# Optimization experiments

Hardware: AMD Instinct MI355X
Metric: run time of the kernel (lower is better)

## Reference

```python
import jax, jax.numpy as jnp
import numpy as np

N = 8192
INP_DIM = 512
OUT_DIM = 256


def setup_inputs() -> dict:
    key = jax.random.key(0)
    k1, k2, k3, k4, k5 = jax.random.split(key, 5)
    x = jax.random.normal(k1, (N, INP_DIM), dtype=jnp.float32)
    adj = jax.random.uniform(k2, (N, N), dtype=jnp.float32)  # threshold at 0.5 below
    # learned params: w ~ torch.rand(inp_dim, out_dim); Linear(out_dim, out_dim)
    w = jax.random.uniform(k3, (INP_DIM, OUT_DIM), dtype=jnp.float32)
    bound = 1.0 / np.sqrt(OUT_DIM)
    lin_w = jax.random.uniform(k4, (OUT_DIM, OUT_DIM), minval=-bound, maxval=bound, dtype=jnp.float32)
    lin_b = jax.random.uniform(k5, (OUT_DIM,), minval=-bound, maxval=bound, dtype=jnp.float32)
    return {"x": x, "adj": adj, "w": w, "lin_w": lin_w, "lin_b": lin_b}


def reference(x, adj, w, lin_w, lin_b):
    n = adj.shape[0]
    # A = binarize(adj) + I
    A = jnp.where(adj > 0.5, 1.0, 0.0) + jnp.eye(n, dtype=adj.dtype)
    # D is diagonal, so inverse().sqrt() == diag(1/sqrt(deg)); deg >= 1 from self-loops
    d_inv_sqrt = jax.lax.rsqrt(jnp.sum(A, axis=1))  # [N]
    # A_hat = D^{-1/2} A D^{-1/2} as row/col scaling (same math, O(N^2))
    A_hat = A * d_inv_sqrt[:, None] * d_inv_sqrt[None, :]
    # message passing + feature transform
    h = jax.nn.relu((A_hat @ x) @ w)           # [N, out_dim]
    return h @ lin_w.T + lin_b                  # Linear(out_dim, out_dim)
```

## Files before the change

### kernel.cpp

```cpp
#include <hip/hip_runtime.h>
#include <hip/hip_bf16.h>

typedef __attribute__((ext_vector_type(4))) float f32x4;
typedef __attribute__((ext_vector_type(8))) short s16x8;
typedef unsigned int uint;
typedef unsigned short ushort;
typedef unsigned long long u64;


__device__ inline ushort f2bf(float f) {
  union { float f; uint u; } v; v.f = f;
  uint r = (v.u + 0x7FFFu + ((v.u >> 16) & 1u)) >> 16;
  return (ushort)r;
}
__device__ inline float bf2f(ushort h) { union { uint u; float f; } v; v.u = ((uint)h) << 16; return v.f; }
__device__ inline uint pack2(float a, float b) { return (uint)f2bf(a) | ((uint)f2bf(b) << 16); }
__device__ inline int kappa(int j) {
  return (j & ~255) | ((j & 3) << 6) | (((j >> 7) & 1) << 5) | ((j >> 2) & 31);
}
__device__ inline int ikappa(int k) {
  return (k & ~255) | ((k >> 6) & 3) | (((k >> 5) & 1) << 7) | ((k & 31) << 2);
}

__global__ __launch_bounds__(256) void k_pack(const float* __restrict__ adj,
                                              const float* __restrict__ w,
                                              const float* __restrict__ lw,
                                              uint* __restrict__ bits,
                                              float* __restrict__ dinv,
                                              float* __restrict__ dk,
                                              ushort* __restrict__ wT,
                                              ushort* __restrict__ lwb) {
  const int t = threadIdx.x, lane = t & 63, wv = t >> 6;
  const int b = blockIdx.x;
  const int row = b * 4 + wv;
  const f32x4* src = (const f32x4*)(adj + (size_t)row * 8192) + lane;
  uint* dst = bits + (size_t)row * 256;
  f32x4 A[4], B[4], C[4];
#pragma unroll
  for (int j = 0; j < 4; ++j) A[j] = __builtin_nontemporal_load(src + j * 64);
#pragma unroll
  for (int j = 0; j < 4; ++j) B[j] = __builtin_nontemporal_load(src + 256 + j * 64);
  int cnt = 0;
#pragma unroll
  for (int bt = 0; bt < 8; ++bt) {
    if (bt + 2 < 8) {
#pragma unroll
      for (int j = 0; j < 4; ++j)
        C[j] = __builtin_nontemporal_load(src + (bt + 2) * 256 + j * 64);
    }
#pragma unroll
    for (int j = 0; j < 4; ++j) {
      u64 b0 = __ballot(A[j].x > 0.5f), b1 = __ballot(A[j].y > 0.5f);
      u64 b2 = __ballot(A[j].z > 0.5f), b3 = __ballot(A[j].w > 0.5f);
      cnt += __popcll(b0) + __popcll(b1) + __popcll(b2) + __popcll(b3);
      if ((lane & 31) == 0) {
        uint4 v = (lane == 0)
          ? make_uint4((uint)b0, (uint)(b0 >> 32), (uint)b1, (uint)(b1 >> 32))
          : make_uint4((uint)b2, (uint)(b2 >> 32), (uint)b3, (uint)(b3 >> 32));
        *(uint4*)(dst + (bt * 4 + j) * 8 + (lane >> 5) * 4) = v;
      }
    }
#pragma unroll
    for (int j = 0; j < 4; ++j) { A[j] = B[j]; B[j] = C[j]; }
  }
  if (lane == 0) {
    float d = rsqrtf((float)(cnt + 1));
    dinv[row] = d;
    dk[kappa(row)] = d;
  }
  if (b < 256) {
#pragma unroll
    for (int kk = 0; kk < 2; ++kk) {
      int k = b * 2 + kk;
      wT[(size_t)t * 512 + k] = f2bf(w[(size_t)k * 256 + t]);
    }
  } else if (b < 288) {
    const int b2 = b - 256;
    const float4* s = (const float4*)lw + b2 * 512;
    uint2* d = (uint2*)lwb + b2 * 512;
#pragma unroll
    for (int ii = 0; ii < 2; ++ii) {
      float4 v = s[ii * 256 + t];
      uint2 p; p.x = pack2(v.x, v.y); p.y = pack2(v.z, v.w);
      d[ii * 256 + t] = p;
    }
  }
}

__global__ __launch_bounds__(512) void k_xw(const float* __restrict__ x,
                                            const ushort* __restrict__ wT,
                                            const float* __restrict__ dk,
                                            ushort* __restrict__ PB,
                                            ushort* __restrict__ zRow) {
  __shared__ ushort xa[2][32 * 64];
  __shared__ ushort zs[32 * 264];
  const int b = blockIdx.x;
  const int bp = (b & 3) * 64 + (b >> 2);
  const int t = threadIdx.x;
  const int lane = t & 63, wid = t >> 6;
  const int mg = wid >> 2, ng = wid & 3;
  const int rl = lane & 15, kg = lane >> 4;
  const int srow = t >> 4, sseg = t & 15;
  const int jrow = ((bp >> 3) << 8) + ((bp & 1) << 7) + ((bp >> 1) & 3) + srow * 4;
  const float4* xsrc = (const float4*)(x + (size_t)jrow * 512) + sseg;
  const int swb = (sseg * 8) ^ ((srow & 7) << 4);
  const int arow = mg * 16 + rl;
  float4 xv[8];
#pragma unroll
  for (int kc2 = 0; kc2 < 8; kc2++) xv[kc2] = xsrc[kc2 * 16];

  f32x4 acc[4];
#pragma unroll
  for (int q = 0; q < 4; q++) acc[q] = (f32x4){0.f, 0.f, 0.f, 0.f};

  {
    uint2 pk; pk.x = pack2(xv[0].x, xv[0].y); pk.y = pack2(xv[0].z, xv[0].w);
    *(uint2*)((char*)xa[0] + srow * 128 + swb) = pk;
  }
#pragma unroll
  for (int kc2 = 0; kc2 < 8; kc2++) {
    __syncthreads();
    if (kc2 < 7) {
      uint2 pk; pk.x = pack2(xv[kc2 + 1].x, xv[kc2 + 1].y);
      pk.y = pack2(xv[kc2 + 1].z, xv[kc2 + 1].w);
      *(uint2*)((char*)xa[(kc2 + 1) & 1] + srow * 128 + swb) = pk;
    }
#pragma unroll
    for (int ks = 0; ks < 2; ks++) {
      union { uint4 u; s16x8 s; } av;
      av.u = *(uint4*)((char*)xa[kc2 & 1] + arow * 128 + ((ks * 64 + kg * 16) ^ ((rl & 7) << 4)));
#pragma unroll
      for (int q = 0; q < 4; q++) {
        int n = ng * 64 + q * 16 + rl;
        union { uint4 u; s16x8 s; } bv;
        bv.u = *(const uint4*)(wT + (size_t)n * 512 + kc2 * 64 + ks * 32 + kg * 8);
        acc[q] = __builtin_amdgcn_mfma_f32_16x16x32_bf16(av.s, bv.s, acc[q], 0, 0, 0);
      }
    }
  }
  const int kb = bp * 32 + mg * 16 + kg * 4;
  float4 dk4 = *(const float4*)(dk + kb);
  const float dkv[4] = {dk4.x, dk4.y, dk4.z, dk4.w};
  char* pb0 = (char*)PB + (size_t)bp * 16384 + (mg * 2 + (kg >> 1)) * 256 + rl * 16 + (kg & 1) * 8;
  const int kk0 = mg * 16 + kg * 4;
#pragma unroll
  for (int q = 0; q < 4; q++) {
    int n = ng * 64 + q * 16 + rl;
    ushort zu[4];
#pragma unroll
    for (int r = 0; r < 4; r++) zu[r] = f2bf(acc[q][r] * dkv[r]);
    uint2 p;
    p.x = (uint)zu[0] | ((uint)zu[1] << 16);
    p.y = (uint)zu[2] | ((uint)zu[3] << 16);
    *(uint2*)(pb0 + (ng * 4 + q) * 1024) = p;
#pragma unroll
    for (int r = 0; r < 4; r++) zs[(kk0 + r) * 264 + n] = zu[r];
  }
  __syncthreads();
  {
    const int rr = t >> 4, seg = t & 15;
    uint4 v0 = *(uint4*)&zs[rr * 264 + seg * 16];
    uint4 v1 = *(uint4*)&zs[rr * 264 + seg * 16 + 8];
    ushort* dstz = zRow + (size_t)ikappa(bp * 32 + rr) * 256 + seg * 16;
    *(uint4*)dstz = v0;
    *(uint4*)(dstz + 8) = v1;
  }
}

__global__ __launch_bounds__(512) void k_spmm(const uint* __restrict__ bits,
                                              const ushort* __restrict__ PB,
                                              ushort* __restrict__ part2) {
  __shared__ uint4 blds4[128 * 16];
  __shared__ uint2 lut[16];
  const int bx = blockIdx.x;
  const int kc = bx & 3, mb = bx >> 2;
  const int m0 = mb * 128;
  const int t = threadIdx.x;
  const int lane = t & 63, wid = t >> 6;
  const int mg = wid >> 2, ng = wid & 3;
  const int rl = lane & 15, kg = lane >> 4;
  if (t < 16) {
    uint2 e;
    e.x = ((t & 1u) ? 0x3F80u : 0u) | ((t & 2u) ? 0x3F800000u : 0u);
    e.y = ((t & 4u) ? 0x3F80u : 0u) | ((t & 8u) ? 0x3F800000u : 0u);
    lut[t] = e;
  }
  {
    const int r = t >> 2, p = t & 3;
    const uint4* src = (const uint4*)(bits + (size_t)(m0 + r) * 256 + kc * 64);
#pragma unroll
    for (int i = 0; i < 4; ++i) {
      int g = p * 4 + i;
      blds4[r * 16 + (g ^ (r & 15))] = src[g];
    }
  }
  const char* zb0 = (const char*)PB + (size_t)kc * 64 * 16384 + ng * 4096 + kg * 256 + rl * 16;
  __syncthreads();

  uint4 bufA[4], bufB[4];
#pragma unroll
  for (int q = 0; q < 4; ++q) bufA[q] = *(const uint4*)(zb0 + q * 1024);

  f32x4 acc[4][4];
#pragma unroll
  for (int f = 0; f < 4; ++f)
#pragma unroll
    for (int q = 0; q < 4; ++q) acc[f][q] = (f32x4){0.f, 0.f, 0.f, 0.f};

  int abase[4];
#pragma unroll
  for (int f = 0; f < 4; ++f) abase[f] = (mg * 64 + f * 16 + rl) * 16;
  const int axor = rl;
  const uint shft = kg * 8;

  for (int a = 0; a < 16; ++a) {
    uint4 aw[4];
#pragma unroll
    for (int f = 0; f < 4; ++f) aw[f] = blds4[abase[f] + (a ^ axor)];
#pragma unroll
    for (int s = 0; s < 4; ++s) {
      const int ks = a * 4 + s;
      const uint4* use = (s & 1) ? bufB : bufA;
      uint4* nxt = (s & 1) ? bufA : bufB;
      if (ks < 63) {
#pragma unroll
        for (int q = 0; q < 4; ++q)
          nxt[q] = *(const uint4*)(zb0 + (size_t)(ks + 1) * 16384 + q * 1024);
      }
#pragma unroll
      for (int f = 0; f < 4; ++f) {
        uint wrd = (s == 0) ? aw[f].x : (s == 1) ? aw[f].y : (s == 2) ? aw[f].z : aw[f].w;
        uint byt = (wrd >> shft) & 0xFFu;
        uint2 lo = lut[byt & 0xFu];
        uint2 hi = lut[byt >> 4];
        union { uint4 u; s16x8 s8; } au;
        au.u = make_uint4(lo.x, lo.y, hi.x, hi.y);
#pragma unroll
        for (int q = 0; q < 4; ++q) {
          union { uint4 u; s16x8 s8; } bu; bu.u = use[q];
          acc[f][q] = __builtin_amdgcn_mfma_f32_16x16x32_bf16(au.s8, bu.s8, acc[f][q], 0, 0, 0);
        }
      }
    }
  }
#pragma unroll
  for (int f = 0; f < 4; ++f)
#pragma unroll
    for (int q = 0; q < 4; ++q) {
      int n = ng * 64 + q * 16 + rl;
      int mt = mb * 4 + mg * 2 + (f >> 1);
      int moff = (f & 1) * 16 + kg * 4;
      uint2 p;
      p.x = pack2(acc[f][q][0], acc[f][q][1]);
      p.y = pack2(acc[f][q][2], acc[f][q][3]);
      *(uint2*)(part2 + ((((size_t)mt * 4 + kc) * 256 + n) * 32 + moff)) = p;
    }
}

__global__ __launch_bounds__(512) void k_lin(const ushort* __restrict__ part2,
                                             const ushort* __restrict__ zRow,
                                             const float* __restrict__ dinv,
                                             const ushort* __restrict__ lwb,
                                             const float* __restrict__ lb,
                                             float* __restrict__ out) {
  __shared__ ushort hA[32 * 256];
  __shared__ float sdinv[32];
  const int m0 = blockIdx.x * 32;
  const int t = threadIdx.x;
  if (t < 32) sdinv[t] = dinv[m0 + t];
  {
    const int n = t & 255, mh = t >> 8;
    float sum[16];
#pragma unroll
    for (int j = 0; j < 16; ++j)
      sum[j] = bf2f(zRow[(size_t)(m0 + mh * 16 + j) * 256 + n]);
#pragma unroll
    for (int kcp = 0; kcp < 4; kcp++) {
      const ushort* pp = part2 + (((size_t)blockIdx.x * 4 + kcp) * 256 + n) * 32 + mh * 16;
      uint4 pa = *(const uint4*)pp, pbq = *(const uint4*)(pp + 8);
      uint pu[8] = {pa.x, pa.y, pa.z, pa.w, pbq.x, pbq.y, pbq.z, pbq.w};
#pragma unroll
      for (int i = 0; i < 8; i++) {
        sum[2 * i]     += bf2f((ushort)(pu[i] & 0xFFFF));
        sum[2 * i + 1] += bf2f((ushort)(pu[i] >> 16));
      }
    }
    __syncthreads();
#pragma unroll
    for (int j = 0; j < 16; j++) {
      int m = mh * 16 + j;
      float h = sum[j] * sdinv[m];
      h = h > 0.f ? h : 0.f;
      *(ushort*)((char*)hA + m * 512 + ((n * 2) ^ ((m & 7) << 4))) = f2bf(h);
    }
  }
  __syncthreads();
  const int lane = t & 63, wid = t >> 6;
  const int rl = lane & 15, kg = lane >> 4;
  f32x4 acc[2][2];
#pragma unroll
  for (int f = 0; f < 2; f++)
#pragma unroll
    for (int q = 0; q < 2; q++) acc[f][q] = (f32x4){0.f, 0.f, 0.f, 0.f};

#pragma unroll
  for (int ks = 0; ks < 8; ks++) {
    union { uint4 u; s16x8 s; } av[2];
#pragma unroll
    for (int f = 0; f < 2; f++)
      av[f].u = *(uint4*)((char*)hA + (f * 16 + rl) * 512 + ((ks * 64 + kg * 16) ^ ((rl & 7) << 4)));
#pragma unroll
    for (int q = 0; q < 2; q++) {
      int no = wid * 32 + q * 16 + rl;
      union { uint4 u; s16x8 s; } bv;
      bv.u = *(const uint4*)(lwb + (size_t)no * 256 + ks * 32 + kg * 8);
#pragma unroll
      for (int f = 0; f < 2; f++)
        acc[f][q] = __builtin_amdgcn_mfma_f32_16x16x32_bf16(av[f].s, bv.s, acc[f][q], 0, 0, 0);
    }
  }
#pragma unroll
  for (int q = 0; q < 2; q++) {
    int no = wid * 32 + q * 16 + rl;
    float bb = lb[no];
#pragma unroll
    for (int f = 0; f < 2; f++) {
      int mbase = m0 + f * 16 + kg * 4;
#pragma unroll
      for (int r = 0; r < 4; r++)
        out[(size_t)(mbase + r) * 256 + no] = acc[f][q][r] + bb;
    }
  }
}

extern "C" void kernel_launch(void* const* d_in, const int* in_sizes, int n_in,
                              void* d_out, int out_size, void* d_ws, size_t ws_size,
                              hipStream_t stream) {
  const float* x   = (const float*)d_in[0];
  const float* adj = (const float*)d_in[1];
  const float* w   = (const float*)d_in[2];
  const float* lw  = (const float*)d_in[3];
  const float* lb  = (const float*)d_in[4];
  float* out = (float*)d_out;

  char* ws = (char*)d_ws;
  float*  dinv  = (float*)(ws + 0);
  float*  dk    = (float*)(ws + (32u << 10));
  ushort* lwb   = (ushort*)(ws + (128u << 10));
  ushort* wT    = (ushort*)(ws + (256u << 10));
  uint*   bits  = (uint*)(ws + (1ull << 20));
  ushort* PB    = (ushort*)(ws + (9ull << 20));
  ushort* part2 = (ushort*)(ws + (16ull << 20));
  ushort* zRow  = (ushort*)(ws + (48ull << 20));

  hipLaunchKernelGGL(k_pack, dim3(2048), dim3(256), 0, stream, adj, w, lw, bits, dinv, dk, wT, lwb);
  hipLaunchKernelGGL(k_xw, dim3(256), dim3(512), 0, stream, x, wT, dk, PB, zRow);
  hipLaunchKernelGGL(k_spmm, dim3(256), dim3(512), 0, stream, bits, PB, part2);
  hipLaunchKernelGGL(k_lin, dim3(256), dim3(512), 0, stream, part2, zRow, dinv, lwb, lb, out);
}
```

Measured before the change: 118.6 us.

## Stage B tiles through double-buffered shared memory instead of per-wave global loads

Rather than having each wave fetch its own B fragments from global memory into registers, the 512-thread block now cooperatively loads each 16KB B k-slice into a double-buffered LDS stage and every wave reads its fragments from LDS. Each slice is loaded once per block, not once per mg wave-group, which halves global/L2 traffic for B. The cost is an extra LDS write and read per element and a block-wide __syncthreads on every one of the 64 k-steps, which can stall the MFMA pipeline. It also adds 32KB of LDS, which may reduce occupancy.

```diff
diff --git a/kernel.cpp b/kernel.cpp
--- a/kernel.cpp
+++ b/kernel.cpp
@@ -171,6 +171,7 @@
                                               const ushort* __restrict__ PB,
                                               ushort* __restrict__ part2) {
   __shared__ uint4 blds4[128 * 16];
+  __shared__ uint4 bstage[2][1024];
   __shared__ uint2 lut[16];
   const int bx = blockIdx.x;
   const int kc = bx & 3, mb = bx >> 2;
@@ -194,12 +195,12 @@
       blds4[r * 16 + (g ^ (r & 15))] = src[g];
     }
   }
-  const char* zb0 = (const char*)PB + (size_t)kc * 64 * 16384 + ng * 4096 + kg * 256 + rl * 16;
+  const uint4* zg = (const uint4*)((const char*)PB + (size_t)kc * 64 * 16384);
+  {
+    bstage[0][t * 2] = zg[t * 2];
+    bstage[0][t * 2 + 1] = zg[t * 2 + 1];
+  }
   __syncthreads();
-
-  uint4 bufA[4], bufB[4];
-#pragma unroll
-  for (int q = 0; q < 4; ++q) bufA[q] = *(const uint4*)(zb0 + q * 1024);
 
   f32x4 acc[4][4];
 #pragma unroll
@@ -212,36 +213,45 @@
   for (int f = 0; f < 4; ++f) abase[f] = (mg * 64 + f * 16 + rl) * 16;
   const int axor = rl;
   const uint shft = kg * 8;
-
-  for (int a = 0; a < 16; ++a) {
-    uint4 aw[4];
-#pragma unroll
-    for (int f = 0; f < 4; ++f) aw[f] = blds4[abase[f] + (a ^ axor)];
-#pragma unroll
-    for (int s = 0; s < 4; ++s) {
-      const int ks = a * 4 + s;
-      const uint4* use = (s & 1) ? bufB : bufA;
-      uint4* nxt = (s & 1) ? bufA : bufB;
-      if (ks < 63) {
-#pragma unroll
-        for (int q = 0; q < 4; ++q)
-          nxt[q] = *(const uint4*)(zb0 + (size_t)(ks + 1) * 16384 + q * 1024);
+  const int boff = ng * 256 + kg * 16 + rl;
+
+  uint4 aw[4];
+  for (int ks = 0; ks < 64; ++ks) {
+    const int cur = ks & 1;
+    const bool more = (ks < 63);
+    uint4 va, vb;
+    if (more) {
+      va = zg[(size_t)(ks + 1) * 1024 + t * 2];
+      vb = zg[(size_t)(ks + 1) * 1024 + t * 2 + 1];
+    }
+    if ((ks & 3) == 0) {
+      const int a = ks >> 2;
+#pragma unroll
+      for (int f = 0; f < 4; ++f) aw[f] = blds4[abase[f] + (a ^ axor)];
+    }
+    const int s = ks & 3;
+    uint4 bu[4];
+#pragma unroll
+    for (int q = 0; q < 4; ++q) bu[q] = bstage[cur][q * 64 + boff];
+#pragma unroll
+    for (int f = 0; f < 4; ++f) {
+      uint wrd = (s == 0) ? aw[f].x : (s == 1) ? aw[f].y : (s == 2) ? aw[f].z : aw[f].w;
+      uint byt = (wrd >> shft) & 0xFFu;
+      uint2 lo = lut[byt & 0xFu];
+      uint2 hi = lut[byt >> 4];
+      union { uint4 u; s16x8 s8; } au;
+      au.u = make_uint4(lo.x, lo.y, hi.x, hi.y);
+#pragma unroll
+      for (int q = 0; q < 4; ++q) {
+        union { uint4 u; s16x8 s8; } b2; b2.u = bu[q];
+        acc[f][q] = __builtin_amdgcn_mfma_f32_16x16x32_bf16(au.s8, b2.s8, acc[f][q], 0, 0, 0);
       }
-#pragma unroll
-      for (int f = 0; f < 4; ++f) {
-        uint wrd = (s == 0) ? aw[f].x : (s == 1) ? aw[f].y : (s == 2) ? aw[f].z : aw[f].w;
-        uint byt = (wrd >> shft) & 0xFFu;
-        uint2 lo = lut[byt & 0xFu];
-        uint2 hi = lut[byt >> 4];
-        union { uint4 u; s16x8 s8; } au;
-        au.u = make_uint4(lo.x, lo.y, hi.x, hi.y);
-#pragma unroll
-        for (int q = 0; q < 4; ++q) {
-          union { uint4 u; s16x8 s8; } bu; bu.u = use[q];
-          acc[f][q] = __builtin_amdgcn_mfma_f32_16x16x32_bf16(au.s8, bu.s8, acc[f][q], 0, 0, 0);
-        }
-      }
-    }
+    }
+    if (more) {
+      bstage[cur ^ 1][t * 2] = va;
+      bstage[cur ^ 1][t * 2 + 1] = vb;
+    }
+    __syncthreads();
   }
 #pragma unroll
   for (int f = 0; f < 4; ++f)
```

New measurement: 129.1 us. 1.09x slower.

## Switch SpMM inner loop from 16x16x32 to 32x32x16 bf16 MFMA tiles

Applied to the files above, without the earlier changes.

Restructures the adjacency-times-features kernel to use 32x32x16 MFMA instructions, with 2x2 accumulator fragments per wave instead of 4x4 16x16 fragments. Each loaded B fragment and each decoded bitmask A fragment now feeds more MACs, which cuts LDS lookups, bit decoding and global B loads per flop. The K loop is split into 128 half-steps with a remapped B addressing and a remapped output store layout. The cost is a reindexing that must exactly match the packed B layout and the part2 layout.

```diff
diff --git a/kernel.cpp b/kernel.cpp
--- a/kernel.cpp
+++ b/kernel.cpp
@@ -2,6 +2,7 @@
 #include <hip/hip_bf16.h>
 
 typedef __attribute__((ext_vector_type(4))) float f32x4;
+typedef __attribute__((ext_vector_type(16))) float f32x16;
 typedef __attribute__((ext_vector_type(8))) short s16x8;
 typedef unsigned int uint;
 typedef unsigned short ushort;
@@ -178,7 +179,7 @@
   const int t = threadIdx.x;
   const int lane = t & 63, wid = t >> 6;
   const int mg = wid >> 2, ng = wid & 3;
-  const int rl = lane & 15, kg = lane >> 4;
+  const int l31 = lane & 31, hi = lane >> 5, l15 = lane & 15;
   if (t < 16) {
     uint2 e;
     e.x = ((t & 1u) ? 0x3F80u : 0u) | ((t & 2u) ? 0x3F800000u : 0u);
@@ -194,66 +195,80 @@
       blds4[r * 16 + (g ^ (r & 15))] = src[g];
     }
   }
-  const char* zb0 = (const char*)PB + (size_t)kc * 64 * 16384 + ng * 4096 + kg * 256 + rl * 16;
+  const char* pbase = (const char*)PB + (size_t)kc * 64 * 16384;
+  int bb[2];
+#pragma unroll
+  for (int nf = 0; nf < 2; ++nf) {
+    int n = ng * 64 + nf * 32 + l31;
+    bb[nf] = (n >> 4) * 1024 + l15 * 16 + hi * 256;
+  }
+  int arow[2];
+#pragma unroll
+  for (int mf = 0; mf < 2; ++mf) arow[mf] = (mg * 64 + mf * 32 + l31) * 16;
+
+  uint4 bufA[2], bufB[2];
+#pragma unroll
+  for (int nf = 0; nf < 2; ++nf) bufA[nf] = *(const uint4*)(pbase + bb[nf]);
   __syncthreads();
 
-  uint4 bufA[4], bufB[4];
-#pragma unroll
-  for (int q = 0; q < 4; ++q) bufA[q] = *(const uint4*)(zb0 + q * 1024);
-
-  f32x4 acc[4][4];
-#pragma unroll
-  for (int f = 0; f < 4; ++f)
-#pragma unroll
-    for (int q = 0; q < 4; ++q) acc[f][q] = (f32x4){0.f, 0.f, 0.f, 0.f};
-
-  int abase[4];
-#pragma unroll
-  for (int f = 0; f < 4; ++f) abase[f] = (mg * 64 + f * 16 + rl) * 16;
-  const int axor = rl;
-  const uint shft = kg * 8;
-
-  for (int a = 0; a < 16; ++a) {
-    uint4 aw[4];
-#pragma unroll
-    for (int f = 0; f < 4; ++f) aw[f] = blds4[abase[f] + (a ^ axor)];
-#pragma unroll
-    for (int s = 0; s < 4; ++s) {
-      const int ks = a * 4 + s;
-      const uint4* use = (s & 1) ? bufB : bufA;
-      uint4* nxt = (s & 1) ? bufA : bufB;
-      if (ks < 63) {
-#pragma unroll
-        for (int q = 0; q < 4; ++q)
-          nxt[q] = *(const uint4*)(zb0 + (size_t)(ks + 1) * 16384 + q * 1024);
-      }
-#pragma unroll
-      for (int f = 0; f < 4; ++f) {
-        uint wrd = (s == 0) ? aw[f].x : (s == 1) ? aw[f].y : (s == 2) ? aw[f].z : aw[f].w;
-        uint byt = (wrd >> shft) & 0xFFu;
+  f32x16 acc[2][2];
+#pragma unroll
+  for (int mf = 0; mf < 2; ++mf)
+#pragma unroll
+    for (int nf = 0; nf < 2; ++nf)
+#pragma unroll
+      for (int r = 0; r < 16; ++r) acc[mf][nf][r] = 0.f;
+
+  const int hshift = hi * 8;
+  uint4 aw[2];
+  for (int ga = 0; ga < 16; ++ga) {
+#pragma unroll
+    for (int mf = 0; mf < 2; ++mf) aw[mf] = blds4[arow[mf] + (ga ^ l15)];
+#pragma unroll
+    for (int s = 0; s < 8; ++s) {
+      const int ks = ga * 8 + s;
+      const uint4* use = (ks & 1) ? bufB : bufA;
+      uint4* nxt = (ks & 1) ? bufA : bufB;
+      if (ks < 127) {
+        const int ks1 = ks + 1;
+        const size_t off = (size_t)(ks1 >> 1) * 16384 + (ks1 & 1) * 512;
+#pragma unroll
+        for (int nf = 0; nf < 2; ++nf)
+          nxt[nf] = *(const uint4*)(pbase + off + bb[nf]);
+      }
+      union { uint4 u; s16x8 s8; } af[2];
+#pragma unroll
+      for (int mf = 0; mf < 2; ++mf) {
+        uint word = (s >> 1) == 0 ? aw[mf].x : (s >> 1) == 1 ? aw[mf].y
+                  : (s >> 1) == 2 ? aw[mf].z : aw[mf].w;
+        uint byt = (word >> ((s & 1) * 16 + hshift)) & 0xFFu;
         uint2 lo = lut[byt & 0xFu];
-        uint2 hi = lut[byt >> 4];
-        union { uint4 u; s16x8 s8; } au;
-        au.u = make_uint4(lo.x, lo.y, hi.x, hi.y);
-#pragma unroll
-        for (int q = 0; q < 4; ++q) {
-          union { uint4 u; s16x8 s8; } bu; bu.u = use[q];
-          acc[f][q] = __builtin_amdgcn_mfma_f32_16x16x32_bf16(au.s8, bu.s8, acc[f][q], 0, 0, 0);
+        uint2 h2 = lut[byt >> 4];
+        af[mf].u = make_uint4(lo.x, lo.y, h2.x, h2.y);
+      }
+#pragma unroll
+      for (int mf = 0; mf < 2; ++mf)
+#pragma unroll
+        for (int nf = 0; nf < 2; ++nf) {
+          union { uint4 u; s16x8 s8; } bu; bu.u = use[nf];
+          acc[mf][nf] = __builtin_amdgcn_mfma_f32_32x32x16_bf16(af[mf].s8, bu.s8, acc[mf][nf], 0, 0, 0);
         }
-      }
-    }
-  }
-#pragma unroll
-  for (int f = 0; f < 4; ++f)
-#pragma unroll
-    for (int q = 0; q < 4; ++q) {
-      int n = ng * 64 + q * 16 + rl;
-      int mt = mb * 4 + mg * 2 + (f >> 1);
-      int moff = (f & 1) * 16 + kg * 4;
-      uint2 p;
-      p.x = pack2(acc[f][q][0], acc[f][q][1]);
-      p.y = pack2(acc[f][q][2], acc[f][q][3]);
-      *(uint2*)(part2 + ((((size_t)mt * 4 + kc) * 256 + n) * 32 + moff)) = p;
+    }
+  }
+#pragma unroll
+  for (int mf = 0; mf < 2; ++mf)
+#pragma unroll
+    for (int nf = 0; nf < 2; ++nf) {
+      const int mt = mb * 4 + mg * 2 + mf;
+      const int n = ng * 64 + nf * 32 + l31;
+      ushort* base = part2 + (((size_t)mt * 4 + kc) * 256 + n) * 32;
+#pragma unroll
+      for (int q4 = 0; q4 < 4; ++q4) {
+        uint2 p;
+        p.x = pack2(acc[mf][nf][q4 * 4 + 0], acc[mf][nf][q4 * 4 + 1]);
+        p.y = pack2(acc[mf][nf][q4 * 4 + 2], acc[mf][nf][q4 * 4 + 3]);
+        *(uint2*)(base + q4 * 8 + hi * 4) = p;
+      }
     }
 }
 
```

Result: no change. 118.7 us, median of 2 (+0.1%).
